# Kernel optimization log

Measured on AMD Instinct MI355X. Metric: run time of the kernel, lower is better.

## Reference

```python
import jax, jax.numpy as jnp
import numpy as np

N, E, IN, H1, H2 = 100000, 3200000, 128, 64, 64


def setup_inputs() -> dict:
    key = jax.random.key(0)
    ks = jax.random.split(key, 6)
    return {
        "edge_index": jax.random.randint(ks[0], (2, E), 0, N),
        "edge_weight": jax.random.uniform(ks[1], (E,), jnp.float32),
        "emb": jax.random.normal(ks[2], (N, IN), jnp.float32) * 0.05,  # xavier-initialized node embeddings
        "W1": jax.random.normal(ks[3], (IN, H1), jnp.float32) / np.sqrt(IN),
        "b1": jnp.zeros((H1,), jnp.float32),
        "W2": jax.random.normal(ks[4], (H1, H2), jnp.float32) / np.sqrt(H1),
        "b2": jnp.zeros((H2,), jnp.float32),
    }


def _digcn_conv(x, edge_index, edge_weight, W, b):
    # DIGCNConv: dense transform, then weighted sparse neighborhood sum-aggregation.
    x = x @ W                                              # [N, d_out]
    msg = edge_weight[:, None] * x[edge_index[0]]          # gather sources -> [E, d_out]
    out = jax.ops.segment_sum(msg, edge_index[1], num_segments=x.shape[0])  # scatter-add to targets
    return out + b


def reference(edge_index, edge_weight, emb, W1, b1, W2, b2):
    h = jax.nn.relu(_digcn_conv(emb, edge_index, edge_weight, W1, b1))
    # F.dropout with training=False is identity (inference mode)
    return _digcn_conv(h, edge_index, edge_weight, W2, b2)
```

## Files before the change

### kernel.cpp

```cpp
#include <hip/hip_runtime.h>
#include <hip/hip_bf16.h>

#define NNODES 100000
#define DIN 128
#define DH 64
#define SRCMASK 0x1FFFF
#define BSH2 8
#define BN2 256
#define NBUCK2 ((NNODES + BN2 - 1) >> BSH2)
#define NCAP 9088
#define EPB 8192
#define MAXBLK 512
#define OVFCAP 4096

typedef short s16x8 __attribute__((ext_vector_type(8)));
typedef float f32x4 __attribute__((ext_vector_type(4)));

static __device__ __forceinline__ short f2bf(float f) {
  __hip_bfloat16 h = __float2bfloat16(f);
  return *reinterpret_cast<short*>(&h);
}
static __device__ __forceinline__ float bf2f(short s) {
  return __uint_as_float(((unsigned)(unsigned short)s) << 16);
}


__global__ __launch_bounds__(256, 4) void gemm1_mfma(
    const float* __restrict__ emb, const float* __restrict__ W1,
    __hip_bfloat16* __restrict__ x1, int N) {
  __shared__ short Bhi[4 * 4 * 64 * 8];
  __shared__ short Blo[4 * 4 * 64 * 8];
  int tid = threadIdx.x;

  for (int idx = tid; idx < 8192; idx += 256) {
    int i = idx & 7, ln = (idx >> 3) & 63, ct = (idx >> 9) & 3, kc = idx >> 11;
    int k = kc * 32 + (ln >> 4) * 8 + i;
    int col = ct * 16 + (ln & 15);
    float w = W1[k * DH + col];
    short h = f2bf(w);
    Bhi[idx] = h;
    Blo[idx] = f2bf(w - bf2f(h));
  }
  __syncthreads();

  int lane = tid & 63, wv = tid >> 6;
  int r0 = (blockIdx.x * 8 + wv * 2) * 16;
  if (r0 >= N) return;

  const int rA = lane & 15, g = lane >> 4;
  f32x4 acc[2][4] = {};

#pragma unroll
  for (int kc = 0; kc < 4; ++kc) {
    s16x8 ahi[2], alo[2];
#pragma unroll
    for (int rt = 0; rt < 2; ++rt) {
      int r = r0 + rt * 16 + rA;
      float av[8];
      if (r < N) {
        const float4* ap = (const float4*)(emb + (long)r * DIN + kc * 32 + g * 8);
        float4 v0 = ap[0], v1 = ap[1];
        av[0] = v0.x; av[1] = v0.y; av[2] = v0.z; av[3] = v0.w;
        av[4] = v1.x; av[5] = v1.y; av[6] = v1.z; av[7] = v1.w;
      } else {
#pragma unroll
        for (int i = 0; i < 8; ++i) av[i] = 0.f;
      }
#pragma unroll
      for (int i = 0; i < 8; ++i) {
        short h = f2bf(av[i]);
        ahi[rt][i] = h;
        alo[rt][i] = f2bf(av[i] - bf2f(h));
      }
    }
#pragma unroll
    for (int ct = 0; ct < 4; ++ct) {
      int fo = ((kc * 4 + ct) * 64 + lane) * 8;
      s16x8 bh = *(const s16x8*)&Bhi[fo];
      s16x8 bl = *(const s16x8*)&Blo[fo];
#pragma unroll
      for (int rt = 0; rt < 2; ++rt) {
        acc[rt][ct] = __builtin_amdgcn_mfma_f32_16x16x32_bf16(ahi[rt], bh, acc[rt][ct], 0, 0, 0);
        acc[rt][ct] = __builtin_amdgcn_mfma_f32_16x16x32_bf16(alo[rt], bh, acc[rt][ct], 0, 0, 0);
        acc[rt][ct] = __builtin_amdgcn_mfma_f32_16x16x32_bf16(ahi[rt], bl, acc[rt][ct], 0, 0, 0);
      }
    }
  }

#pragma unroll
  for (int rt = 0; rt < 2; ++rt) {
#pragma unroll
    for (int j = 0; j < 4; ++j) {
      int row = r0 + rt * 16 + g * 4 + j;
      if (row < N) {
#pragma unroll
        for (int ct = 0; ct < 4; ++ct)
          x1[(long)row * DH + ct * 16 + rA] = __float2bfloat16(acc[rt][ct][j]);
      }
    }
  }
}

__global__ __launch_bounds__(256, 4) void gemm2_mfma(
    const float* __restrict__ agg, const float* __restrict__ W2,
    const float* __restrict__ b1, __hip_bfloat16* __restrict__ x2, int N) {
  __shared__ short Bhi[2 * 4 * 64 * 8];
  __shared__ short Blo[2 * 4 * 64 * 8];
  int tid = threadIdx.x;

  for (int idx = tid; idx < 4096; idx += 256) {
    int i = idx & 7, ln = (idx >> 3) & 63, ct = (idx >> 9) & 3, kc = (idx >> 11) & 1;
    int k = kc * 32 + (ln >> 4) * 8 + i;
    int col = ct * 16 + (ln & 15);
    float w = W2[k * DH + col];
    short h = f2bf(w);
    Bhi[idx] = h;
    Blo[idx] = f2bf(w - bf2f(h));
  }
  __syncthreads();

  int lane = tid & 63, wv = tid >> 6;
  int r0 = (blockIdx.x * 8 + wv * 2) * 16;
  if (r0 >= N) return;

  const int rA = lane & 15, g = lane >> 4;
  f32x4 acc[2][4] = {};

#pragma unroll
  for (int kc = 0; kc < 2; ++kc) {
    const float4* bp = (const float4*)(b1 + kc * 32 + g * 8);
    float4 b0 = bp[0], b4 = bp[1];
    float bv[8] = {b0.x, b0.y, b0.z, b0.w, b4.x, b4.y, b4.z, b4.w};
    s16x8 ahi[2], alo[2];
#pragma unroll
    for (int rt = 0; rt < 2; ++rt) {
      int r = r0 + rt * 16 + rA;
      float av[8];
      if (r < N) {
        const float4* ap = (const float4*)(agg + (long)r * DH + kc * 32 + g * 8);
        float4 v0 = ap[0], v1 = ap[1];
        av[0] = v0.x; av[1] = v0.y; av[2] = v0.z; av[3] = v0.w;
        av[4] = v1.x; av[5] = v1.y; av[6] = v1.z; av[7] = v1.w;
      } else {
#pragma unroll
        for (int i = 0; i < 8; ++i) av[i] = -1e30f;
      }
#pragma unroll
      for (int i = 0; i < 8; ++i) {
        float a = fmaxf(av[i] + bv[i], 0.f);
        short h = f2bf(a);
        ahi[rt][i] = h;
        alo[rt][i] = f2bf(a - bf2f(h));
      }
    }
#pragma unroll
    for (int ct = 0; ct < 4; ++ct) {
      int fo = ((kc * 4 + ct) * 64 + lane) * 8;
      s16x8 bh = *(const s16x8*)&Bhi[fo];
      s16x8 bl = *(const s16x8*)&Blo[fo];
#pragma unroll
      for (int rt = 0; rt < 2; ++rt) {
        acc[rt][ct] = __builtin_amdgcn_mfma_f32_16x16x32_bf16(ahi[rt], bh, acc[rt][ct], 0, 0, 0);
        acc[rt][ct] = __builtin_amdgcn_mfma_f32_16x16x32_bf16(alo[rt], bh, acc[rt][ct], 0, 0, 0);
        acc[rt][ct] = __builtin_amdgcn_mfma_f32_16x16x32_bf16(ahi[rt], bl, acc[rt][ct], 0, 0, 0);
      }
    }
  }

#pragma unroll
  for (int rt = 0; rt < 2; ++rt) {
#pragma unroll
    for (int j = 0; j < 4; ++j) {
      int row = r0 + rt * 16 + g * 4 + j;
      if (row < N) {
#pragma unroll
        for (int ct = 0; ct < 4; ++ct)
          x2[(long)row * DH + ct * 16 + rA] = __float2bfloat16(acc[rt][ct][j]);
      }
    }
  }
}

__global__ __launch_bounds__(512) void block_sort(
    const int* __restrict__ srcs, const int* __restrict__ dsts,
    const float* __restrict__ w, int2* __restrict__ sorted,
    unsigned short* __restrict__ offTab, int E) {
  __shared__ int2 stage[EPB];
  __shared__ int hist[512];
  __shared__ int sc[512];
  __shared__ int cur[512];
  int tid = threadIdx.x, blk = blockIdx.x;
  int e0 = blk * EPB;

  hist[tid] = 0;
  __syncthreads();

  int pk[16], bd[16];
#pragma unroll
  for (int i = 0; i < 16; ++i) {
    int e = e0 + i * 512 + tid;
    if (e < E) {
      int s = srcs[e], d = dsts[e];
      float wv = w[e];
      int q = (int)(wv * 32768.f + 0.5f);
      if (q > 32767) q = 32767;
      pk[i] = (s & SRCMASK) | (q << 17);
      bd[i] = d;
    } else bd[i] = -1;
  }
#pragma unroll
  for (int i = 0; i < 16; ++i)
    if (bd[i] >= 0) atomicAdd(&hist[bd[i] >> BSH2], 1);
  __syncthreads();

  sc[tid] = (tid < NBUCK2) ? hist[tid] : 0;
  __syncthreads();
  for (int d = 1; d < 512; d <<= 1) {
    int u = (tid >= d) ? sc[tid - d] : 0;
    __syncthreads();
    sc[tid] += u;
    __syncthreads();
  }
  long row = (long)blk * (NBUCK2 + 1);
  if (tid < NBUCK2) {
    int base = sc[tid] - hist[tid];
    cur[tid] = base;
    offTab[row + tid] = (unsigned short)base;
    if (tid == NBUCK2 - 1) offTab[row + NBUCK2] = (unsigned short)sc[tid];
  }
  __syncthreads();

#pragma unroll
  for (int i = 0; i < 16; ++i) {
    if (bd[i] >= 0) {
      int pos = atomicAdd(&cur[bd[i] >> BSH2], 1);
      stage[pos] = make_int2(pk[i], bd[i] & (BN2 - 1));
    }
  }
  __syncthreads();

  int eN = min(EPB, E - e0);
  for (int i = tid; i < eN; i += 512)
    sorted[(long)blk * EPB + i] = stage[i];
}

__global__ __launch_bounds__(512) void gather_build(
    const unsigned short* __restrict__ offTab, const int2* __restrict__ sorted,
    int* __restrict__ noff, int* __restrict__ ndeg, int* __restrict__ pairs,
    int2* __restrict__ ovf, int* __restrict__ ovfcnt, int NBLK, int N) {
  __shared__ int2 gath[NCAP];
  __shared__ unsigned short offR[MAXBLK];
  __shared__ unsigned short cntR[MAXBLK];
  __shared__ int baseR[MAXBLK];
  __shared__ int sc[512];
  __shared__ int deg[BN2], cur[BN2];
  int b = blockIdx.x, tid = threadIdx.x;

  for (int blk = tid; blk < NBLK; blk += 512) {
    long row = (long)blk * (NBUCK2 + 1);
    int st = offTab[row + b];
    int en = offTab[row + b + 1];
    offR[blk] = (unsigned short)st;
    cntR[blk] = (unsigned short)(en - st);
  }
  __syncthreads();

  sc[tid] = (tid < NBLK) ? (int)cntR[tid] : 0;
  __syncthreads();
  for (int d = 1; d < 512; d <<= 1) {
    int u = (tid >= d) ? sc[tid - d] : 0;
    __syncthreads();
    sc[tid] += u;
    __syncthreads();
  }
  if (tid < NBLK) baseR[tid] = sc[tid] - (int)cntR[tid];
  __syncthreads();
  int total = sc[NBLK - 1];
  int tcl = total > NCAP ? NCAP : total;

  int wv = tid >> 6, lane = tid & 63;
  for (int blk = wv; blk < NBLK; blk += 8) {
    int st = offR[blk], c = cntR[blk], gb = baseR[blk];
    for (int l = lane; l < c; l += 64) {
      int2 v = sorted[(long)blk * EPB + st + l];
      int gp = gb + l;
      if (gp < NCAP) gath[gp] = v;
      else {
        int oi = atomicAdd(ovfcnt, 1);
        if (oi < OVFCAP) ovf[oi] = make_int2(v.x, (b << BSH2) | v.y);
      }
    }
  }
  if (tid < BN2) deg[tid] = 0;
  __syncthreads();

  for (int k = tid; k < tcl; k += 512)
    atomicAdd(&deg[gath[k].y & (BN2 - 1)], 1);
  __syncthreads();

  sc[tid] = (tid < BN2) ? deg[tid] : 0;
  __syncthreads();
  for (int d = 1; d < 512; d <<= 1) {
    int u = (tid >= d) ? sc[tid - d] : 0;
    __syncthreads();
    sc[tid] += u;
    __syncthreads();
  }
  if (tid < BN2) {
    int excl = sc[tid] - deg[tid];
    int gpos = b * NCAP + excl;
    cur[tid] = gpos;
    int n = (b << BSH2) + tid;
    if (n < N) { noff[n] = gpos; ndeg[n] = deg[tid]; }
  }
  __syncthreads();

  for (int k = tid; k < tcl; k += 512) {
    int p = atomicAdd(&cur[gath[k].y & (BN2 - 1)], 1);
    pairs[p] = gath[k].x;
  }
}

__global__ __launch_bounds__(256) void ovf_fixup(
    const int2* __restrict__ ovf, const int* __restrict__ ovfcnt,
    const short* __restrict__ x, float* __restrict__ out) {
  int cnt = *ovfcnt;
  if (cnt > OVFCAP) cnt = OVFCAP;
  int wid = (int)((blockIdx.x * 256 + threadIdx.x) >> 6);
  int lane = threadIdx.x & 63;
  int nw = (gridDim.x * 256) >> 6;
  for (int i = wid; i < cnt; i += nw) {
    int2 e = ovf[i];
    unsigned p = (unsigned)e.x;
    float wv = (float)(p >> 17) * (1.f / 32768.f);
    float xv = bf2f(x[(long)(p & SRCMASK) * DH + lane]);
    atomicAdd(&out[(long)e.y * DH + lane], wv * xv);
  }
}

#define ACC4(P, XV)                                          \
  do {                                                       \
    float wv_ = (float)((P) >> 17) * (1.f / 32768.f);        \
    a0 += wv_ * __uint_as_float((XV).x << 16);               \
    a1 += wv_ * __uint_as_float((XV).x & 0xFFFF0000u);       \
    a2 += wv_ * __uint_as_float((XV).y << 16);               \
    a3 += wv_ * __uint_as_float((XV).y & 0xFFFF0000u);       \
  } while (0)

__global__ __launch_bounds__(256) void agg_quad(
    const int* __restrict__ pairs, const int* __restrict__ noff,
    const int* __restrict__ ndeg,
    const uint2* __restrict__ x,
    const float* __restrict__ bias, float* __restrict__ out, int N) {
  int wid = (int)(((long)blockIdx.x * 256 + threadIdx.x) >> 6);
  int lane = threadIdx.x & 63;
  if (wid >= N) return;
  int h = lane >> 4;
  int fj = lane & 15;
  int st = noff[wid];
  int m = ndeg[wid];
  float a0 = 0.f, a1 = 0.f, a2 = 0.f, a3 = 0.f;

  for (int base = 0; base < m; base += 64) {
    int pl = (base + lane < m) ? pairs[st + base + lane] : 0;
    int mm = m - base;

    unsigned pg[8];
#pragma unroll
    for (int g = 0; g < 8; ++g) pg[g] = (unsigned)__shfl(pl, g * 4 + h);
    uint2 xg[8];
#pragma unroll
    for (int g = 0; g < 8; ++g) xg[g] = x[(pg[g] & SRCMASK) * 16 + fj];
#pragma unroll
    for (int g = 0; g < 8; ++g) ACC4(pg[g], xg[g]);

#pragma unroll
    for (int q = 32; q < 64; q += 16) {
      if (q >= mm) break;
      unsigned p0 = (unsigned)__shfl(pl, q + h);
      unsigned p1 = (unsigned)__shfl(pl, q + 4 + h);
      unsigned p2 = (unsigned)__shfl(pl, q + 8 + h);
      unsigned p3 = (unsigned)__shfl(pl, q + 12 + h);
      uint2 y0 = x[(p0 & SRCMASK) * 16 + fj];
      uint2 y1 = x[(p1 & SRCMASK) * 16 + fj];
      uint2 y2 = x[(p2 & SRCMASK) * 16 + fj];
      uint2 y3 = x[(p3 & SRCMASK) * 16 + fj];
      ACC4(p0, y0); ACC4(p1, y1); ACC4(p2, y2); ACC4(p3, y3);
    }
  }

  a0 += __shfl_xor(a0, 16); a0 += __shfl_xor(a0, 32);
  a1 += __shfl_xor(a1, 16); a1 += __shfl_xor(a1, 32);
  a2 += __shfl_xor(a2, 16); a2 += __shfl_xor(a2, 32);
  a3 += __shfl_xor(a3, 16); a3 += __shfl_xor(a3, 32);
  if (lane < 16) {
    if (bias) {
      float4 bv = ((const float4*)bias)[fj];
      a0 += bv.x; a1 += bv.y; a2 += bv.z; a3 += bv.w;
    }
    ((float4*)out)[(long)wid * 16 + fj] = make_float4(a0, a1, a2, a3);
  }
}


__global__ __launch_bounds__(256) void gemm1_f32(
    const float* __restrict__ emb, const float* __restrict__ W1,
    float* __restrict__ x1, int N) {
  __shared__ float Ws[DIN * DH];
  __shared__ float rows[4][DIN];
  int tid = threadIdx.x;
  for (int i = tid; i < DIN * DH; i += 256) Ws[i] = W1[i];
  int r0 = blockIdx.x * 4;
  for (int i = tid; i < 4 * DIN; i += 256) {
    int rr = i >> 7, kk = i & 127;
    int r = r0 + rr;
    rows[rr][kk] = (r < N) ? emb[(long)r * DIN + kk] : 0.f;
  }
  __syncthreads();
  int rr = tid >> 6, j = tid & 63;
  int r = r0 + rr;
  float acc = 0.f;
#pragma unroll
  for (int k = 0; k < DIN; ++k) acc += rows[rr][k] * Ws[k * DH + j];
  if (r < N) x1[(long)r * DH + j] = acc;
}

__global__ __launch_bounds__(256) void gemm2_f32(
    const float* __restrict__ agg, const float* __restrict__ W2,
    const float* __restrict__ b1, float* __restrict__ x2, int N) {
  __shared__ float Ws[DH * DH];
  __shared__ float rows[4][DH];
  int tid = threadIdx.x;
  for (int i = tid; i < DH * DH; i += 256) Ws[i] = W2[i];
  int r0 = blockIdx.x * 4;
  {
    int rr = tid >> 6, kk = tid & 63;
    int r = r0 + rr;
    float v = (r < N) ? agg[(long)r * DH + kk] + b1[kk] : 0.f;
    rows[rr][kk] = v > 0.f ? v : 0.f;
  }
  __syncthreads();
  int rr = tid >> 6, j = tid & 63;
  float acc = 0.f;
#pragma unroll
  for (int k = 0; k < DH; ++k) acc += rows[rr][k] * Ws[k * DH + j];
  int r = r0 + rr;
  if (r < N) x2[(long)r * DH + j] = acc;
}

__global__ __launch_bounds__(256) void init_bias_kernel(
    float* __restrict__ out, const float* __restrict__ b2, int total) {
  int i = blockIdx.x * 256 + threadIdx.x;
  if (i < total) out[i] = b2[i & 63];
}

__global__ __launch_bounds__(256) void scatter_kernel(
    const int* __restrict__ srcs, const int* __restrict__ dsts,
    const float* __restrict__ w, const float* __restrict__ x,
    float* __restrict__ out, int E) {
  long t = (long)blockIdx.x * 256 + threadIdx.x;
  long e = t >> 6;
  if (e >= E) return;
  int j = (int)(t & 63);
  int s = srcs[e];
  int d = dsts[e];
  float val = w[e] * x[(long)s * DH + j];
  atomicAdd(&out[(long)d * DH + j], val);
}


static inline size_t align256(size_t x) { return (x + 255) & ~(size_t)255; }

extern "C" void kernel_launch(void* const* d_in, const int* in_sizes, int n_in,
                              void* d_out, int out_size, void* d_ws, size_t ws_size,
                              hipStream_t stream) {
  const int*   edge_index = (const int*)d_in[0];
  const float* edge_w     = (const float*)d_in[1];
  const float* emb        = (const float*)d_in[2];
  const float* b1         = (const float*)d_in[4];
  const float* W1         = (const float*)d_in[3];
  const float* W2         = (const float*)d_in[5];
  const float* b2         = (const float*)d_in[6];
  float* out = (float*)d_out;

  const int E = in_sizes[0] / 2;
  const int N = NNODES;
  const int* srcs = edge_index;
  const int* dsts = edge_index + E;

  const int NBLK = (E + EPB - 1) / EPB;

  const size_t sortedbytes = (size_t)NBLK * EPB * sizeof(int2);
  const size_t xbytes_bf   = (size_t)N * DH * sizeof(__hip_bfloat16);
  const size_t offTabbytes = (size_t)NBLK * (NBUCK2 + 1) * sizeof(unsigned short);
  const size_t pairsbytes  = (size_t)NBUCK2 * NCAP * sizeof(int);
  const size_t nbytes      = (size_t)N * sizeof(int);

  const int aggBlocks = (N + 3) / 4;
  const int gemmBlocks = (N + 127) / 128;

  size_t off = 0;
  char* base = (char*)d_ws;
  int2* sorted = (int2*)(base + off);
  off = align256(off + (sortedbytes > xbytes_bf ? sortedbytes : xbytes_bf));
  __hip_bfloat16* xbuf = (__hip_bfloat16*)sorted;
  unsigned short* offTab = (unsigned short*)(base + off); off = align256(off + offTabbytes);
  int* pairs = (int*)(base + off);  off = align256(off + pairsbytes);
  int* noff  = (int*)(base + off);  off = align256(off + nbytes);
  int* ndeg  = (int*)(base + off);  off = align256(off + nbytes);
  int2* ovf  = (int2*)(base + off); off = align256(off + OVFCAP * sizeof(int2));
  int* ovfcnt = (int*)(base + off); off = align256(off + 256);
  const size_t needed_full = off;

  if (ws_size >= needed_full && NBLK <= MAXBLK) {
    hipMemsetAsync(ovfcnt, 0, sizeof(int), stream);
    block_sort<<<NBLK, 512, 0, stream>>>(srcs, dsts, edge_w, sorted, offTab, E);
    gather_build<<<NBUCK2, 512, 0, stream>>>(offTab, sorted, noff, ndeg, pairs,
                                             ovf, ovfcnt, NBLK, N);

    gemm1_mfma<<<gemmBlocks, 256, 0, stream>>>(emb, W1, xbuf, N);
    agg_quad<<<aggBlocks, 256, 0, stream>>>(pairs, noff, ndeg, (const uint2*)xbuf,
                                            nullptr, out, N);
    ovf_fixup<<<8, 256, 0, stream>>>(ovf, ovfcnt, (const short*)xbuf, out);

    gemm2_mfma<<<gemmBlocks, 256, 0, stream>>>(out, W2, b1, xbuf, N);
    agg_quad<<<aggBlocks, 256, 0, stream>>>(pairs, noff, ndeg, (const uint2*)xbuf,
                                            b2, out, N);
    ovf_fixup<<<8, 256, 0, stream>>>(ovf, ovfcnt, (const short*)xbuf, out);
    return;
  }

  const long scatterThreads = (long)E * 64;
  const int scatterBlocks = (int)((scatterThreads + 255) / 256);
  const int rowBlocks4 = (N + 3) / 4;
  float* xb1 = (float*)d_ws;

  gemm1_f32<<<rowBlocks4, 256, 0, stream>>>(emb, W1, xb1, N);
  hipMemsetAsync(d_out, 0, (size_t)N * DH * sizeof(float), stream);
  scatter_kernel<<<scatterBlocks, 256, 0, stream>>>(srcs, dsts, edge_w, xb1, out, E);

  gemm2_f32<<<rowBlocks4, 256, 0, stream>>>(out, W2, b1, xb1, N);
  init_bias_kernel<<<(N * DH + 255) / 256, 256, 0, stream>>>(out, b2, N * DH);
  scatter_kernel<<<scatterBlocks, 256, 0, stream>>>(srcs, dsts, edge_w, xb1, out, E);
}
```

Baseline: 200.8 us.

## Process four nodes per wave in aggregation with software-pipelined neighbor gathers

The aggregation kernel now assigns four destination nodes to each wavefront instead of one. While the current node is being accumulated, it prefetches the first 32 neighbor feature rows of the next node, which overlaps gather latency across nodes and amortizes the per-node metadata loads. The launch grid shrinks fourfold to match. The cost is higher register pressure from the extra buffered gathers, which may lower occupancy.

```diff
diff --git a/kernel.cpp b/kernel.cpp
--- a/kernel.cpp
+++ b/kernel.cpp
@@ -180,6 +180,7 @@
     }
   }
 }
+
 
 __global__ __launch_bounds__(512) void block_sort(
     const int* __restrict__ srcs, const int* __restrict__ dsts,
@@ -352,53 +353,90 @@
     const int* __restrict__ ndeg,
     const uint2* __restrict__ x,
     const float* __restrict__ bias, float* __restrict__ out, int N) {
-  int wid = (int)(((long)blockIdx.x * 256 + threadIdx.x) >> 6);
+  int wv = (int)(((long)blockIdx.x * 256 + threadIdx.x) >> 6);
   int lane = threadIdx.x & 63;
-  if (wid >= N) return;
   int h = lane >> 4;
   int fj = lane & 15;
-  int st = noff[wid];
-  int m = ndeg[wid];
-  float a0 = 0.f, a1 = 0.f, a2 = 0.f, a3 = 0.f;
-
-  for (int base = 0; base < m; base += 64) {
-    int pl = (base + lane < m) ? pairs[st + base + lane] : 0;
-    int mm = m - base;
-
-    unsigned pg[8];
-#pragma unroll
-    for (int g = 0; g < 8; ++g) pg[g] = (unsigned)__shfl(pl, g * 4 + h);
-    uint2 xg[8];
-#pragma unroll
-    for (int g = 0; g < 8; ++g) xg[g] = x[(pg[g] & SRCMASK) * 16 + fj];
-#pragma unroll
-    for (int g = 0; g < 8; ++g) ACC4(pg[g], xg[g]);
-
-#pragma unroll
-    for (int q = 32; q < 64; q += 16) {
-      if (q >= mm) break;
-      unsigned p0 = (unsigned)__shfl(pl, q + h);
-      unsigned p1 = (unsigned)__shfl(pl, q + 4 + h);
-      unsigned p2 = (unsigned)__shfl(pl, q + 8 + h);
-      unsigned p3 = (unsigned)__shfl(pl, q + 12 + h);
-      uint2 y0 = x[(p0 & SRCMASK) * 16 + fj];
-      uint2 y1 = x[(p1 & SRCMASK) * 16 + fj];
-      uint2 y2 = x[(p2 & SRCMASK) * 16 + fj];
-      uint2 y3 = x[(p3 & SRCMASK) * 16 + fj];
-      ACC4(p0, y0); ACC4(p1, y1); ACC4(p2, y2); ACC4(p3, y3);
-    }
-  }
-
-  a0 += __shfl_xor(a0, 16); a0 += __shfl_xor(a0, 32);
-  a1 += __shfl_xor(a1, 16); a1 += __shfl_xor(a1, 32);
-  a2 += __shfl_xor(a2, 16); a2 += __shfl_xor(a2, 32);
-  a3 += __shfl_xor(a3, 16); a3 += __shfl_xor(a3, 32);
-  if (lane < 16) {
-    if (bias) {
-      float4 bv = ((const float4*)bias)[fj];
-      a0 += bv.x; a1 += bv.y; a2 += bv.z; a3 += bv.w;
-    }
-    ((float4*)out)[(long)wid * 16 + fj] = make_float4(a0, a1, a2, a3);
+  int n0 = wv * 4;
+  if (n0 >= N) return;
+
+  int pl[4], st[4], m[4];
+#pragma unroll
+  for (int j = 0; j < 4; ++j) {
+    int n = n0 + j;
+    st[j] = (n < N) ? noff[n] : 0;
+    m[j]  = (n < N) ? ndeg[n] : 0;
+  }
+#pragma unroll
+  for (int j = 0; j < 4; ++j)
+    pl[j] = (lane < m[j]) ? pairs[st[j] + lane] : 0;
+
+  unsigned pgA[8], pgB[8], pgC[8];
+  uint2 xgA[8], xgB[8], xgC[8];
+#pragma unroll
+  for (int g = 0; g < 8; ++g) pgA[g] = (unsigned)__shfl(pl[0], g * 4 + h);
+#pragma unroll
+  for (int g = 0; g < 8; ++g) xgA[g] = x[(pgA[g] & SRCMASK) * 16 + fj];
+
+#pragma unroll
+  for (int j = 0; j < 4; ++j) {
+    if (j + 1 < 4) {
+#pragma unroll
+      for (int g = 0; g < 8; ++g) pgB[g] = (unsigned)__shfl(pl[j + 1], g * 4 + h);
+#pragma unroll
+      for (int g = 0; g < 8; ++g) xgB[g] = x[(pgB[g] & SRCMASK) * 16 + fj];
+    }
+    bool big = (m[j] > 32);
+    if (big) {
+#pragma unroll
+      for (int g = 0; g < 8; ++g) pgC[g] = (unsigned)__shfl(pl[j], 32 + g * 4 + h);
+#pragma unroll
+      for (int g = 0; g < 8; ++g) xgC[g] = x[(pgC[g] & SRCMASK) * 16 + fj];
+    }
+
+    float a0 = 0.f, a1 = 0.f, a2 = 0.f, a3 = 0.f;
+#pragma unroll
+    for (int g = 0; g < 8; ++g) ACC4(pgA[g], xgA[g]);
+    if (big) {
+#pragma unroll
+      for (int g = 0; g < 8; ++g) ACC4(pgC[g], xgC[g]);
+    }
+
+    if (m[j] > 64) {
+      for (int base = 64; base < m[j]; base += 64) {
+        int pls = (base + lane < m[j]) ? pairs[st[j] + base + lane] : 0;
+        int mm = m[j] - base;
+        for (int q = 0; q < 64; q += 16) {
+          if (q >= mm) break;
+          unsigned p0 = (unsigned)__shfl(pls, q + h);
+          unsigned p1 = (unsigned)__shfl(pls, q + 4 + h);
+          unsigned p2 = (unsigned)__shfl(pls, q + 8 + h);
+          unsigned p3 = (unsigned)__shfl(pls, q + 12 + h);
+          uint2 y0 = x[(p0 & SRCMASK) * 16 + fj];
+          uint2 y1 = x[(p1 & SRCMASK) * 16 + fj];
+          uint2 y2 = x[(p2 & SRCMASK) * 16 + fj];
+          uint2 y3 = x[(p3 & SRCMASK) * 16 + fj];
+          ACC4(p0, y0); ACC4(p1, y1); ACC4(p2, y2); ACC4(p3, y3);
+        }
+      }
+    }
+
+    a0 += __shfl_xor(a0, 16); a0 += __shfl_xor(a0, 32);
+    a1 += __shfl_xor(a1, 16); a1 += __shfl_xor(a1, 32);
+    a2 += __shfl_xor(a2, 16); a2 += __shfl_xor(a2, 32);
+    a3 += __shfl_xor(a3, 16); a3 += __shfl_xor(a3, 32);
+    if (lane < 16 && n0 + j < N) {
+      if (bias) {
+        float4 bv = ((const float4*)bias)[fj];
+        a0 += bv.x; a1 += bv.y; a2 += bv.z; a3 += bv.w;
+      }
+      ((float4*)out)[(long)(n0 + j) * 16 + fj] = make_float4(a0, a1, a2, a3);
+    }
+
+    if (j + 1 < 4) {
+#pragma unroll
+      for (int g = 0; g < 8; ++g) { pgA[g] = pgB[g]; xgA[g] = xgB[g]; }
+    }
   }
 }
 
@@ -477,8 +515,8 @@
   const int*   edge_index = (const int*)d_in[0];
   const float* edge_w     = (const float*)d_in[1];
   const float* emb        = (const float*)d_in[2];
+  const float* W1         = (const float*)d_in[3];
   const float* b1         = (const float*)d_in[4];
-  const float* W1         = (const float*)d_in[3];
   const float* W2         = (const float*)d_in[5];
   const float* b2         = (const float*)d_in[6];
   float* out = (float*)d_out;
@@ -496,7 +534,7 @@
   const size_t pairsbytes  = (size_t)NBUCK2 * NCAP * sizeof(int);
   const size_t nbytes      = (size_t)N * sizeof(int);
 
-  const int aggBlocks = (N + 3) / 4;
+  const int aggBlocks = (N + 15) / 16;
   const int gemmBlocks = (N + 127) / 128;
 
   size_t off = 0;
```

Measured after the change: 203.8 us. No clear change (+1.5%).

## Fuse edge block-sort and first GEMM into one heterogeneous launch

Applied to the files above, without the earlier changes.

Combines the edge bucket sort and the first dense transform into a single kernel whose extra blocks run the MFMA GEMM, so the two independent stages share the GPU at once and one launch plus the ovfcnt memset are removed (a designated block zeroes the counter). This requires separate workspace for the sorted edges and the bf16 feature buffer, which previously aliased, so the old aliased layout is kept as a fallback path when workspace is smaller. The GEMM blocks now cover 256 rows with 512 threads and rebuild split bf16 hi/lo W1 fragments in shared memory. The risk is the larger combined shared-memory footprint and uneven load between sort and GEMM blocks.

```diff
diff --git a/kernel.cpp b/kernel.cpp
--- a/kernel.cpp
+++ b/kernel.cpp
@@ -181,6 +181,7 @@
   }
 }
 
+
 __global__ __launch_bounds__(512) void block_sort(
     const int* __restrict__ srcs, const int* __restrict__ dsts,
     const float* __restrict__ w, int2* __restrict__ sorted,
@@ -190,6 +191,149 @@
   __shared__ int sc[512];
   __shared__ int cur[512];
   int tid = threadIdx.x, blk = blockIdx.x;
+  int e0 = blk * EPB;
+
+  hist[tid] = 0;
+  __syncthreads();
+
+  int pk[16], bd[16];
+#pragma unroll
+  for (int i = 0; i < 16; ++i) {
+    int e = e0 + i * 512 + tid;
+    if (e < E) {
+      int s = srcs[e], d = dsts[e];
+      float wv = w[e];
+      int q = (int)(wv * 32768.f + 0.5f);
+      if (q > 32767) q = 32767;
+      pk[i] = (s & SRCMASK) | (q << 17);
+      bd[i] = d;
+    } else bd[i] = -1;
+  }
+#pragma unroll
+  for (int i = 0; i < 16; ++i)
+    if (bd[i] >= 0) atomicAdd(&hist[bd[i] >> BSH2], 1);
+  __syncthreads();
+
+  sc[tid] = (tid < NBUCK2) ? hist[tid] : 0;
+  __syncthreads();
+  for (int d = 1; d < 512; d <<= 1) {
+    int u = (tid >= d) ? sc[tid - d] : 0;
+    __syncthreads();
+    sc[tid] += u;
+    __syncthreads();
+  }
+  long row = (long)blk * (NBUCK2 + 1);
+  if (tid < NBUCK2) {
+    int base = sc[tid] - hist[tid];
+    cur[tid] = base;
+    offTab[row + tid] = (unsigned short)base;
+    if (tid == NBUCK2 - 1) offTab[row + NBUCK2] = (unsigned short)sc[tid];
+  }
+  __syncthreads();
+
+#pragma unroll
+  for (int i = 0; i < 16; ++i) {
+    if (bd[i] >= 0) {
+      int pos = atomicAdd(&cur[bd[i] >> BSH2], 1);
+      stage[pos] = make_int2(pk[i], bd[i] & (BN2 - 1));
+    }
+  }
+  __syncthreads();
+
+  int eN = min(EPB, E - e0);
+  for (int i = tid; i < eN; i += 512)
+    sorted[(long)blk * EPB + i] = stage[i];
+}
+
+__global__ __launch_bounds__(512, 2) void sort_gemm1(
+    const int* __restrict__ srcs, const int* __restrict__ dsts,
+    const float* __restrict__ w, int2* __restrict__ sorted,
+    unsigned short* __restrict__ offTab, int E,
+    const float* __restrict__ emb, const float* __restrict__ W1,
+    __hip_bfloat16* __restrict__ x1, int N, int NBLK, int* __restrict__ ovfcnt) {
+  __shared__ __align__(16) char smem[EPB * 8 + 3 * 512 * 4];
+  int tid = threadIdx.x;
+
+  if (blockIdx.x >= (unsigned)NBLK) {
+    if (blockIdx.x == (unsigned)NBLK && tid == 0) *ovfcnt = 0;
+    short* Bhi = (short*)smem;
+    short* Blo = Bhi + 8192;
+    for (int idx = tid; idx < 8192; idx += 512) {
+      int i = idx & 7, ln = (idx >> 3) & 63, ct = (idx >> 9) & 3, kc = idx >> 11;
+      int k = kc * 32 + (ln >> 4) * 8 + i;
+      int col = ct * 16 + (ln & 15);
+      float wv = W1[k * DH + col];
+      short h = f2bf(wv);
+      Bhi[idx] = h;
+      Blo[idx] = f2bf(wv - bf2f(h));
+    }
+    __syncthreads();
+
+    int lane = tid & 63, wv8 = tid >> 6;
+    int gblk = blockIdx.x - NBLK;
+    int r0 = gblk * 256 + wv8 * 32;
+    if (r0 >= N) return;
+
+    const int rA = lane & 15, g = lane >> 4;
+    f32x4 acc[2][4] = {};
+
+#pragma unroll
+    for (int kc = 0; kc < 4; ++kc) {
+      s16x8 ahi[2], alo[2];
+#pragma unroll
+      for (int rt = 0; rt < 2; ++rt) {
+        int r = r0 + rt * 16 + rA;
+        float av[8];
+        if (r < N) {
+          const float4* ap = (const float4*)(emb + (long)r * DIN + kc * 32 + g * 8);
+          float4 v0 = ap[0], v1 = ap[1];
+          av[0] = v0.x; av[1] = v0.y; av[2] = v0.z; av[3] = v0.w;
+          av[4] = v1.x; av[5] = v1.y; av[6] = v1.z; av[7] = v1.w;
+        } else {
+#pragma unroll
+          for (int i = 0; i < 8; ++i) av[i] = 0.f;
+        }
+#pragma unroll
+        for (int i = 0; i < 8; ++i) {
+          short h = f2bf(av[i]);
+          ahi[rt][i] = h;
+          alo[rt][i] = f2bf(av[i] - bf2f(h));
+        }
+      }
+#pragma unroll
+      for (int ct = 0; ct < 4; ++ct) {
+        int fo = ((kc * 4 + ct) * 64 + lane) * 8;
+        s16x8 bh = *(const s16x8*)&Bhi[fo];
+        s16x8 bl = *(const s16x8*)&Blo[fo];
+#pragma unroll
+        for (int rt = 0; rt < 2; ++rt) {
+          acc[rt][ct] = __builtin_amdgcn_mfma_f32_16x16x32_bf16(ahi[rt], bh, acc[rt][ct], 0, 0, 0);
+          acc[rt][ct] = __builtin_amdgcn_mfma_f32_16x16x32_bf16(alo[rt], bh, acc[rt][ct], 0, 0, 0);
+          acc[rt][ct] = __builtin_amdgcn_mfma_f32_16x16x32_bf16(ahi[rt], bl, acc[rt][ct], 0, 0, 0);
+        }
+      }
+    }
+
+#pragma unroll
+    for (int rt = 0; rt < 2; ++rt) {
+#pragma unroll
+      for (int j = 0; j < 4; ++j) {
+        int row = r0 + rt * 16 + g * 4 + j;
+        if (row < N) {
+#pragma unroll
+          for (int ct = 0; ct < 4; ++ct)
+            x1[(long)row * DH + ct * 16 + rA] = __float2bfloat16(acc[rt][ct][j]);
+        }
+      }
+    }
+    return;
+  }
+
+  int2* stage = (int2*)smem;
+  int* hist = (int*)(smem + EPB * 8);
+  int* sc   = hist + 512;
+  int* cur  = sc + 512;
+  int blk = blockIdx.x;
   int e0 = blk * EPB;
 
   hist[tid] = 0;
@@ -477,8 +621,8 @@
   const int*   edge_index = (const int*)d_in[0];
   const float* edge_w     = (const float*)d_in[1];
   const float* emb        = (const float*)d_in[2];
+  const float* W1         = (const float*)d_in[3];
   const float* b1         = (const float*)d_in[4];
-  const float* W1         = (const float*)d_in[3];
   const float* W2         = (const float*)d_in[5];
   const float* b2         = (const float*)d_in[6];
   float* out = (float*)d_out;
@@ -498,31 +642,28 @@
 
   const int aggBlocks = (N + 3) / 4;
   const int gemmBlocks = (N + 127) / 128;
+  const int g1Blocks   = (N + 255) / 256;
 
   size_t off = 0;
   char* base = (char*)d_ws;
-  int2* sorted = (int2*)(base + off);
-  off = align256(off + (sortedbytes > xbytes_bf ? sortedbytes : xbytes_bf));
-  __hip_bfloat16* xbuf = (__hip_bfloat16*)sorted;
+  int2* sorted = (int2*)(base + off);              off = align256(off + sortedbytes);
+  __hip_bfloat16* xbuf = (__hip_bfloat16*)(base + off); off = align256(off + xbytes_bf);
   unsigned short* offTab = (unsigned short*)(base + off); off = align256(off + offTabbytes);
   int* pairs = (int*)(base + off);  off = align256(off + pairsbytes);
   int* noff  = (int*)(base + off);  off = align256(off + nbytes);
   int* ndeg  = (int*)(base + off);  off = align256(off + nbytes);
   int2* ovf  = (int2*)(base + off); off = align256(off + OVFCAP * sizeof(int2));
   int* ovfcnt = (int*)(base + off); off = align256(off + 256);
-  const size_t needed_full = off;
-
-  if (ws_size >= needed_full && NBLK <= MAXBLK) {
-    hipMemsetAsync(ovfcnt, 0, sizeof(int), stream);
-    block_sort<<<NBLK, 512, 0, stream>>>(srcs, dsts, edge_w, sorted, offTab, E);
+  const size_t needed_fused = off;
+
+  if (ws_size >= needed_fused && NBLK <= MAXBLK) {
+    sort_gemm1<<<NBLK + g1Blocks, 512, 0, stream>>>(
+        srcs, dsts, edge_w, sorted, offTab, E, emb, W1, xbuf, N, NBLK, ovfcnt);
     gather_build<<<NBUCK2, 512, 0, stream>>>(offTab, sorted, noff, ndeg, pairs,
                                              ovf, ovfcnt, NBLK, N);
-
-    gemm1_mfma<<<gemmBlocks, 256, 0, stream>>>(emb, W1, xbuf, N);
     agg_quad<<<aggBlocks, 256, 0, stream>>>(pairs, noff, ndeg, (const uint2*)xbuf,
                                             nullptr, out, N);
     ovf_fixup<<<8, 256, 0, stream>>>(ovf, ovfcnt, (const short*)xbuf, out);
-
     gemm2_mfma<<<gemmBlocks, 256, 0, stream>>>(out, W2, b1, xbuf, N);
     agg_quad<<<aggBlocks, 256, 0, stream>>>(pairs, noff, ndeg, (const uint2*)xbuf,
                                             b2, out, N);
@@ -530,6 +671,34 @@
     return;
   }
 
+  off = 0;
+  int2* sorted2 = (int2*)(base + off);
+  off = align256(off + (sortedbytes > xbytes_bf ? sortedbytes : xbytes_bf));
+  __hip_bfloat16* xbuf2 = (__hip_bfloat16*)sorted2;
+  unsigned short* offTab2 = (unsigned short*)(base + off); off = align256(off + offTabbytes);
+  int* pairs2 = (int*)(base + off);  off = align256(off + pairsbytes);
+  int* noff2  = (int*)(base + off);  off = align256(off + nbytes);
+  int* ndeg2  = (int*)(base + off);  off = align256(off + nbytes);
+  int2* ovf2  = (int2*)(base + off); off = align256(off + OVFCAP * sizeof(int2));
+  int* ovfcnt2 = (int*)(base + off); off = align256(off + 256);
+  const size_t needed_seq = off;
+
+  if (ws_size >= needed_seq && NBLK <= MAXBLK) {
+    hipMemsetAsync(ovfcnt2, 0, sizeof(int), stream);
+    block_sort<<<NBLK, 512, 0, stream>>>(srcs, dsts, edge_w, sorted2, offTab2, E);
+    gather_build<<<NBUCK2, 512, 0, stream>>>(offTab2, sorted2, noff2, ndeg2, pairs2,
+                                             ovf2, ovfcnt2, NBLK, N);
+    gemm1_mfma<<<gemmBlocks, 256, 0, stream>>>(emb, W1, xbuf2, N);
+    agg_quad<<<aggBlocks, 256, 0, stream>>>(pairs2, noff2, ndeg2, (const uint2*)xbuf2,
+                                            nullptr, out, N);
+    ovf_fixup<<<8, 256, 0, stream>>>(ovf2, ovfcnt2, (const short*)xbuf2, out);
+    gemm2_mfma<<<gemmBlocks, 256, 0, stream>>>(out, W2, b1, xbuf2, N);
+    agg_quad<<<aggBlocks, 256, 0, stream>>>(pairs2, noff2, ndeg2, (const uint2*)xbuf2,
+                                            b2, out, N);
+    ovf_fixup<<<8, 256, 0, stream>>>(ovf2, ovfcnt2, (const short*)xbuf2, out);
+    return;
+  }
+
   const long scatterThreads = (long)E * 64;
   const int scatterBlocks = (int)((scatterThreads + 255) / 256);
   const int rowBlocks4 = (N + 3) / 4;
```

After: 189.4 us. -5.7%, faster.
